# Performance work log

Hardware: AMD Instinct MI355X
Metric: run time of the kernel (lower is better)

The kernel has to match this reference:

```python
import jax, jax.numpy as jnp
import numpy as np

B, S, D_IN, H, D_HEAD = 8, 1024, 768, 12, 64

def setup_inputs() -> dict:
    key = jax.random.key(0)
    k1, k2, k3, k4 = jax.random.split(key, 4)
    x = jax.random.normal(k1, (B, S, D_IN), dtype=jnp.float32)
    # per-head projection weights, stacked: [H, d_in, d_head]
    scale = 1.0 / np.sqrt(D_IN)
    Wq = jax.random.normal(k2, (H, D_IN, D_HEAD), dtype=jnp.float32) * scale
    Wk = jax.random.normal(k3, (H, D_IN, D_HEAD), dtype=jnp.float32) * scale
    Wv = jax.random.normal(k4, (H, D_IN, D_HEAD), dtype=jnp.float32) * scale
    return {"x": x, "Wq": Wq, "Wk": Wk, "Wv": Wv}

def reference(x, Wq, Wk, Wv) -> jnp.ndarray:
    # Batched equivalent of the Python loop over heads + concat.
    q = jnp.einsum('bsd,hde->bhse', x, Wq)  # [B,H,S,Dh]
    k = jnp.einsum('bsd,hde->bhse', x, Wk)
    v = jnp.einsum('bsd,hde->bhse', x, Wv)
    scores = jnp.einsum('bhse,bhte->bhst', q, k) / jnp.sqrt(jnp.asarray(D_HEAD, x.dtype))
    causal = jnp.tril(jnp.ones((S, S), dtype=bool))  # [S,S]
    scores = jnp.where(causal, scores, jnp.asarray(-jnp.inf, x.dtype))
    attn = jax.nn.softmax(scores, axis=-1)  # dropout p=0.0 -> identity
    ctx = jnp.einsum('bhst,bhte->bhse', attn, v)  # [B,H,S,Dh]
    # concat heads along last dim -> [B,S,H*Dh]
    return jnp.transpose(ctx, (0, 2, 1, 3)).reshape(B, S, H * D_HEAD)
```

## Files before the change

kernel.cpp:

```cpp
#include <hip/hip_runtime.h>

typedef short short8 __attribute__((ext_vector_type(8)));
typedef float f32x4 __attribute__((ext_vector_type(4)));
typedef float f32x16 __attribute__((ext_vector_type(16)));

#define SQ   1024
#define DIN  768
#define NH   12
#define DH   64
#define SCL2 0.1803368801111243f

static __device__ __forceinline__ ushort f2bf(float f) {
  union { float f; unsigned u; } v; v.f = f;
  unsigned u = v.u;
  unsigned r = (u + 0x7FFFu + ((u >> 16) & 1u)) >> 16;
  return (ushort)r;
}
static __device__ __forceinline__ unsigned cvtpk(float a, float b) {
  unsigned r;
  asm("v_cvt_pk_bf16_f32 %0, %1, %2" : "=v"(r) : "v"(a), "v"(b));
  return r;
}

static __device__ __forceinline__ void gload_lds16(const ushort* g, ushort* l) {
  __builtin_amdgcn_global_load_lds(
      (const __attribute__((address_space(1))) unsigned*)(g),
      (__attribute__((address_space(3))) unsigned*)(l),
      16, 0, 0);
}

__global__ __launch_bounds__(256) void k_convert_x(const float* __restrict__ x,
                                                   ushort* __restrict__ xb) {
  int i = (blockIdx.x * 256 + threadIdx.x) * 8;
  float4 v0 = *reinterpret_cast<const float4*>(x + i);
  float4 v1 = *reinterpret_cast<const float4*>(x + i + 4);
  uint4 o;
  o.x = cvtpk(v0.x, v0.y); o.y = cvtpk(v0.z, v0.w);
  o.z = cvtpk(v1.x, v1.y); o.w = cvtpk(v1.z, v1.w);
  *reinterpret_cast<uint4*>(xb + i) = o;
}

__global__ __launch_bounds__(256) void k_prep_w(const float* __restrict__ Wq,
                                                const float* __restrict__ Wk,
                                                const float* __restrict__ Wv,
                                                ushort* __restrict__ wt) {
  __shared__ ushort tile[64][65];
  const int mh = blockIdx.x;
  const int m = mh / 12, h = mh % 12;
  const int d0 = blockIdx.y * 64;
  const float* W = (m == 0 ? Wq : (m == 1 ? Wk : Wv)) + h * DIN * DH;
  ushort* outp = wt + (size_t)mh * DH * DIN;
  #pragma unroll
  for (int p = 0; p < 16; ++p) {
    int idx = p * 256 + threadIdx.x;
    int d = idx >> 6, e = idx & 63;
    tile[d][e] = f2bf(W[(d0 + d) * DH + e]);
  }
  __syncthreads();
  #pragma unroll
  for (int p = 0; p < 16; ++p) {
    int idx = p * 256 + threadIdx.x;
    int e = idx >> 6, d = idx & 63;
    outp[e * DIN + d0 + d] = tile[d][e];
  }
}

__global__ __launch_bounds__(256, 2) void k_proj(const ushort* __restrict__ xb,
                                                 const ushort* __restrict__ wt,
                                                 ushort* __restrict__ qo,
                                                 ushort* __restrict__ ko,
                                                 ushort* __restrict__ vto) {
  __shared__ __align__(16) ushort Sb[24576];

  const int brow = blockIdx.x * 256;
  const int bn   = blockIdx.y * 128;
  const int w    = threadIdx.x >> 6, lane = threadIdx.x & 63;
  const int lr   = lane & 15, lg = lane >> 4;
  const int wm   = w >> 1, wn = w & 1;

  const int srow  = threadIdx.x >> 2;
  const int sslot = (threadIdx.x & 3) ^ (srow & 3) ^ ((srow >> 2) & 3);
  const ushort* gA = xb + (size_t)(brow + srow) * DIN + sslot * 8;
  const ushort* gB = wt + (size_t)(bn   + srow) * DIN + sslot * 8;

  f32x4 acc[8][4];
  #pragma unroll
  for (int i = 0; i < 8; ++i)
    #pragma unroll
    for (int j = 0; j < 4; ++j) acc[i][j] = (f32x4){0.f, 0.f, 0.f, 0.f};

  const int fr   = (lr & 3) ^ ((lr >> 2) & 3);
  const int aoff = (lg ^ fr) * 8;

#define STAGEP(bi, tt) do {                                               \
    const int k0_ = (tt) * 32;                                            \
    ushort* la_ = Sb + (bi) * 8192 + threadIdx.x * 8;                     \
    ushort* lb_ = Sb + 16384 + (bi) * 4096 + threadIdx.x * 8;             \
    gload_lds16(gA + k0_,             la_);                               \
    gload_lds16(gA + k0_ +  64 * DIN, la_ + 2048);                        \
    gload_lds16(gA + k0_ + 128 * DIN, la_ + 4096);                        \
    gload_lds16(gA + k0_ + 192 * DIN, la_ + 6144);                        \
    gload_lds16(gB + k0_,             lb_);                               \
    gload_lds16(gB + k0_ +  64 * DIN, lb_ + 2048);                        \
  } while (0)

  STAGEP(0, 0);
  __syncthreads();

  int cur = 0;
  #pragma unroll 1
  for (int t = 0; t < 24; ++t) {
    if (t + 1 < 24) STAGEP(cur ^ 1, t + 1);
    short8 a[8], b[4];
    #pragma unroll
    for (int mi = 0; mi < 8; ++mi)
      a[mi] = *reinterpret_cast<const short8*>(&Sb[cur * 8192 + (wm * 128 + mi * 16 + lr) * 32 + aoff]);
    #pragma unroll
    for (int ci = 0; ci < 4; ++ci)
      b[ci] = *reinterpret_cast<const short8*>(&Sb[16384 + cur * 4096 + (wn * 64 + ci * 16 + lr) * 32 + aoff]);
    #pragma unroll
    for (int mi = 0; mi < 8; ++mi)
      #pragma unroll
      for (int ci = 0; ci < 4; ++ci)
        acc[mi][ci] = __builtin_amdgcn_mfma_f32_16x16x32_bf16(a[mi], b[ci], acc[mi][ci], 0, 0, 0);
    __syncthreads();
    cur ^= 1;
  }
#undef STAGEP

  ushort* ldsw = Sb + w * 4096;
  const int mh = blockIdx.y * 2 + wn;
  const int m = mh / 12, h = mh % 12;
  const int c = lane & 7;

  #pragma unroll
  for (int p = 0; p < 2; ++p) {
    if (m < 2) {
      #pragma unroll
      for (int mi2 = 0; mi2 < 4; ++mi2)
        #pragma unroll
        for (int ci = 0; ci < 4; ++ci)
          #pragma unroll
          for (int r = 0; r < 4; ++r) {
            int sl = mi2 * 16 + lg * 4 + r;
            int e  = ci * 16 + lr;
            ldsw[sl * 64 + (e ^ ((sl & 7) << 3))] = f2bf(acc[p * 4 + mi2][ci][r]);
          }
      asm volatile("s_waitcnt lgkmcnt(0)" ::: "memory");
      ushort* dst = (m == 0) ? qo : ko;
      #pragma unroll
      for (int it = 0; it < 8; ++it) {
        int sl = it * 8 + (lane >> 3);
        short8 vv = *reinterpret_cast<const short8*>(&ldsw[sl * 64 + ((c * 8) ^ ((sl & 7) << 3))]);
        int rg = brow + wm * 128 + p * 64 + sl;
        int b_ = rg >> 10, s_ = rg & 1023;
        *reinterpret_cast<short8*>(dst + ((size_t)(b_ * 12 + h) * SQ + s_) * DH + c * 8) = vv;
      }
    } else {
      #pragma unroll
      for (int mi2 = 0; mi2 < 4; ++mi2)
        #pragma unroll
        for (int ci = 0; ci < 4; ++ci)
          #pragma unroll
          for (int r = 0; r < 4; ++r) {
            int sl = mi2 * 16 + lg * 4 + r;
            int e  = ci * 16 + lr;
            ldsw[e * 64 + (sl ^ ((e & 7) << 3))] = f2bf(acc[p * 4 + mi2][ci][r]);
          }
      asm volatile("s_waitcnt lgkmcnt(0)" ::: "memory");
      #pragma unroll
      for (int it = 0; it < 8; ++it) {
        int e = it * 8 + (lane >> 3);
        short8 vv = *reinterpret_cast<const short8*>(&ldsw[e * 64 + ((c * 8) ^ ((e & 7) << 3))]);
        int rg = brow + wm * 128 + p * 64 + c * 8;
        int b_ = rg >> 10, s_ = rg & 1023;
        *reinterpret_cast<short8*>(vto + ((size_t)(b_ * 12 + h) * DH + e) * SQ + s_) = vv;
      }
    }
  }
}

__global__ __launch_bounds__(256, 3) void k_attn(const ushort* __restrict__ qi,
                                                 const ushort* __restrict__ ki,
                                                 const ushort* __restrict__ vti,
                                                 float* __restrict__ out) {
  __shared__ __align__(16) ushort Kb[2][64 * 64];
  __shared__ __align__(16) ushort Vb[2][64 * 64];

  const int f = blockIdx.x;
  const int g = f >> 8, r_ = f & 255;
  const int qt = ((r_ & 7) + g * 3) & 7;
  const int bh = g * 32 + (r_ >> 3);
  const int b = bh / 12, h = bh % 12;
  const int w = threadIdx.x >> 6, lane = threadIdx.x & 63;
  const int ql = lane & 31, hi = lane >> 5;
  const int q0 = qt * 128 + w * 32;
  const int nt = (q0 >> 6) + 1;
  const int ntmax = 2 * qt + 2;
  const ushort* qb = qi  + (size_t)bh * SQ * DH;
  const ushort* kb = ki  + (size_t)bh * SQ * DH;
  const ushort* vb = vti + (size_t)bh * DH * SQ;

  short8 qf[4];
  #pragma unroll
  for (int m = 0; m < 4; ++m)
    qf[m] = *reinterpret_cast<const short8*>(qb + (size_t)(q0 + ql) * DH + m * 16 + hi * 8);

  f32x16 o0, o1;
  #pragma unroll
  for (int r = 0; r < 16; ++r) { o0[r] = 0.f; o1[r] = 0.f; }
  float m_run = -1e30f, l_run = 0.f;

#define STAGE(bufi, tt) do {                                                                   \
    const int kv0_ = (tt) * 64;                                                                \
    const int t0 = threadIdx.x, t1 = threadIdx.x + 256;                                        \
    gload_lds16(kb + (size_t)(kv0_ + (t0 >> 3)) * DH + (((t0 & 7) ^ ((t0 >> 3) & 7)) * 8),     \
                &Kb[bufi][0] + t0 * 8);                                                        \
    gload_lds16(kb + (size_t)(kv0_ + (t1 >> 3)) * DH + (((t1 & 7) ^ ((t1 >> 3) & 7)) * 8),     \
                &Kb[bufi][0] + t1 * 8);                                                        \
    gload_lds16(vb + (size_t)(t0 >> 3) * SQ + kv0_ + (((t0 & 7) ^ ((t0 >> 3) & 7)) * 8),       \
                &Vb[bufi][0] + t0 * 8);                                                        \
    gload_lds16(vb + (size_t)(t1 >> 3) * SQ + kv0_ + (((t1 & 7) ^ ((t1 >> 3) & 7)) * 8),       \
                &Vb[bufi][0] + t1 * 8);                                                        \
  } while (0)

  STAGE(0, 0);
  __syncthreads();

  int cur = 0;
  #pragma unroll 1
  for (int t = 0; t < ntmax; ++t) {
    if (t + 1 < ntmax) STAGE(cur ^ 1, t + 1);

    if (t < nt) {
      const int kv0 = t * 64;
      const ushort* Kc = &Kb[cur][0];
      const ushort* Vc = &Vb[cur][0];

      f32x16 s0, s1;
      #pragma unroll
      for (int r = 0; r < 16; ++r) { s0[r] = 0.f; s1[r] = 0.f; }
      #pragma unroll
      for (int m = 0; m < 4; ++m) {
        short8 kf = *reinterpret_cast<const short8*>(Kc + ql * 64 + ((2 * m + hi) ^ (ql & 7)) * 8);
        s0 = __builtin_amdgcn_mfma_f32_32x32x16_bf16(kf, qf[m], s0, 0, 0, 0);
      }
      #pragma unroll
      for (int m = 0; m < 4; ++m) {
        short8 kf = *reinterpret_cast<const short8*>(Kc + (32 + ql) * 64 + ((2 * m + hi) ^ (ql & 7)) * 8);
        s1 = __builtin_amdgcn_mfma_f32_32x32x16_bf16(kf, qf[m], s1, 0, 0, 0);
      }

      if (t == nt - 1) {
        const int qg = q0 + ql;
        #pragma unroll
        for (int r = 0; r < 16; ++r) {
          int kvl = (r & 3) + 8 * (r >> 2) + 4 * hi;
          if (kv0 + kvl      > qg) s0[r] = -1e30f;
          if (kv0 + 32 + kvl > qg) s1[r] = -1e30f;
        }
      }

      float mt = s0[0];
      #pragma unroll
      for (int r = 1; r < 16; ++r) mt = fmaxf(mt, s0[r]);
      #pragma unroll
      for (int r = 0; r < 16; ++r) mt = fmaxf(mt, s1[r]);
      mt = fmaxf(mt, __shfl_xor(mt, 32));
      if (__any(mt > m_run + 40.0f)) {
        float mnew = fmaxf(m_run, mt);
        float corr = exp2f((m_run - mnew) * SCL2);
        l_run *= corr; m_run = mnew;
        #pragma unroll
        for (int r = 0; r < 16; ++r) {
          float cr = __shfl(corr, (r & 3) + 8 * (r >> 2) + 4 * hi);
          o0[r] *= cr; o1[r] *= cr;
        }
      }
      float ts = 0.f;
      #pragma unroll
      for (int r = 0; r < 16; ++r) {
        s0[r] = exp2f((s0[r] - m_run) * SCL2); ts += s0[r];
        s1[r] = exp2f((s1[r] - m_run) * SCL2); ts += s1[r];
      }
      ts += __shfl_xor(ts, 32);
      l_run += ts;

#define PV_CHUNK(SV, CC, KC) do {                                                              \
        unsigned wa = cvtpk(SV[(CC) * 8 + 0], SV[(CC) * 8 + 1]);                               \
        unsigned wb = cvtpk(SV[(CC) * 8 + 2], SV[(CC) * 8 + 3]);                               \
        unsigned wc = cvtpk(SV[(CC) * 8 + 4], SV[(CC) * 8 + 5]);                               \
        unsigned wd = cvtpk(SV[(CC) * 8 + 6], SV[(CC) * 8 + 7]);                               \
        unsigned xa = __shfl_xor(wa, 32), xb2 = __shfl_xor(wb, 32);                            \
        unsigned xc = __shfl_xor(wc, 32), xd = __shfl_xor(wd, 32);                             \
        uint4 pw;                                                                              \
        pw.x = hi ? xc : wa;  pw.y = hi ? xd : wb;                                             \
        pw.z = hi ? wc : xa;  pw.w = hi ? wd : xb2;                                            \
        short8 pa = *reinterpret_cast<short8*>(&pw);                                           \
        short8 vf0 = *reinterpret_cast<const short8*>(Vc + ql * 64 +                           \
                       ((2 * (KC) + hi) ^ (ql & 7)) * 8);                                      \
        o0 = __builtin_amdgcn_mfma_f32_32x32x16_bf16(pa, vf0, o0, 0, 0, 0);                    \
        short8 vf1 = *reinterpret_cast<const short8*>(Vc + (32 + ql) * 64 +                    \
                       ((2 * (KC) + hi) ^ (ql & 7)) * 8);                                      \
        o1 = __builtin_amdgcn_mfma_f32_32x32x16_bf16(pa, vf1, o1, 0, 0, 0);                    \
      } while (0)

      PV_CHUNK(s0, 0, 0);
      PV_CHUNK(s0, 1, 1);
      PV_CHUNK(s1, 0, 2);
      PV_CHUNK(s1, 1, 3);
#undef PV_CHUNK
    }

    __syncthreads();
    cur ^= 1;
  }
#undef STAGE

  float rl = 1.0f / l_run;
  #pragma unroll
  for (int r = 0; r < 16; ++r) {
    int base = (r & 3) + 8 * (r >> 2) + 4 * hi;
    float sc_ = __shfl(rl, base);
    int qg = q0 + base;
    float* op = out + ((size_t)b * SQ + qg) * (NH * DH) + h * DH;
    op[ql]      = o0[r] * sc_;
    op[32 + ql] = o1[r] * sc_;
  }
}

extern "C" void kernel_launch(void* const* d_in, const int* in_sizes, int n_in,
                              void* d_out, int out_size, void* d_ws, size_t ws_size,
                              hipStream_t stream) {
  const float* x  = (const float*)d_in[0];
  const float* Wq = (const float*)d_in[1];
  const float* Wk = (const float*)d_in[2];
  const float* Wv = (const float*)d_in[3];
  float* out = (float*)d_out;

  char* ws = (char*)d_ws;
  ushort* xb = (ushort*)(ws);
  ushort* wt = (ushort*)(ws + 12582912);
  ushort* q  = (ushort*)(ws + 16121856);
  ushort* k  = (ushort*)(ws + 28704768);
  ushort* vt = (ushort*)(ws + 41287680);

  k_convert_x<<<3072, 256, 0, stream>>>(x, xb);
  k_prep_w<<<dim3(36, 12), 256, 0, stream>>>(Wq, Wk, Wv, wt);
  k_proj<<<dim3(32, 18), 256, 0, stream>>>(xb, wt, q, k, vt);
  k_attn<<<768, 256, 0, stream>>>(q, k, vt, out);
}
```

Before: 171.3 us.

## Restructure projection GEMM: 128-row tiles, 32x32 MFMA, triple-buffered LDS pipeline

The projection GEMM tile shrinks from 256x128 to 128x128, which doubles the grid to 64x18 blocks for better CU fill. The inner product moves from 16x16x32 to 32x32x16 MFMA instructions. The LDS double buffer becomes a three-stage ring that prefetches two steps ahead, gated by vmcnt waits and a single barrier per iteration. Smaller tiles give less operand reuse per block and more global traffic, traded for more parallelism and latency hiding.

Measured after the change: 169.7 us. About the same (-1.0%).

```diff
diff --git a/kernel.cpp b/kernel.cpp
--- a/kernel.cpp
+++ b/kernel.cpp
@@ -65,17 +65,17 @@
   }
 }
 
-__global__ __launch_bounds__(256, 2) void k_proj(const ushort* __restrict__ xb,
-                                                 const ushort* __restrict__ wt,
-                                                 ushort* __restrict__ qo,
-                                                 ushort* __restrict__ ko,
-                                                 ushort* __restrict__ vto) {
+__global__ __launch_bounds__(256) void k_proj(const ushort* __restrict__ xb,
+                                              const ushort* __restrict__ wt,
+                                              ushort* __restrict__ qo,
+                                              ushort* __restrict__ ko,
+                                              ushort* __restrict__ vto) {
   __shared__ __align__(16) ushort Sb[24576];
 
-  const int brow = blockIdx.x * 256;
+  const int brow = blockIdx.x * 128;
   const int bn   = blockIdx.y * 128;
   const int w    = threadIdx.x >> 6, lane = threadIdx.x & 63;
-  const int lr   = lane & 15, lg = lane >> 4;
+  const int ql   = lane & 31, hi = lane >> 5;
   const int wm   = w >> 1, wn = w & 1;
 
   const int srow  = threadIdx.x >> 2;
@@ -83,99 +83,116 @@
   const ushort* gA = xb + (size_t)(brow + srow) * DIN + sslot * 8;
   const ushort* gB = wt + (size_t)(bn   + srow) * DIN + sslot * 8;
 
-  f32x4 acc[8][4];
-  #pragma unroll
-  for (int i = 0; i < 8; ++i)
-    #pragma unroll
-    for (int j = 0; j < 4; ++j) acc[i][j] = (f32x4){0.f, 0.f, 0.f, 0.f};
-
-  const int fr   = (lr & 3) ^ ((lr >> 2) & 3);
-  const int aoff = (lg ^ fr) * 8;
+  f32x16 acc[2][2];
+  #pragma unroll
+  for (int i = 0; i < 2; ++i)
+    #pragma unroll
+    for (int j = 0; j < 2; ++j)
+      #pragma unroll
+      for (int r = 0; r < 16; ++r) acc[i][j][r] = 0.f;
+
+  const int frq = (ql & 3) ^ ((ql >> 2) & 3);
 
 #define STAGEP(bi, tt) do {                                               \
     const int k0_ = (tt) * 32;                                            \
-    ushort* la_ = Sb + (bi) * 8192 + threadIdx.x * 8;                     \
-    ushort* lb_ = Sb + 16384 + (bi) * 4096 + threadIdx.x * 8;             \
-    gload_lds16(gA + k0_,             la_);                               \
-    gload_lds16(gA + k0_ +  64 * DIN, la_ + 2048);                        \
-    gload_lds16(gA + k0_ + 128 * DIN, la_ + 4096);                        \
-    gload_lds16(gA + k0_ + 192 * DIN, la_ + 6144);                        \
-    gload_lds16(gB + k0_,             lb_);                               \
-    gload_lds16(gB + k0_ +  64 * DIN, lb_ + 2048);                        \
+    ushort* la_ = Sb + (bi) * 4096 + threadIdx.x * 8;                     \
+    ushort* lb_ = Sb + 12288 + (bi) * 4096 + threadIdx.x * 8;             \
+    gload_lds16(gA + k0_,            la_);                                \
+    gload_lds16(gA + k0_ + 64 * DIN, la_ + 2048);                         \
+    gload_lds16(gB + k0_,            lb_);                                \
+    gload_lds16(gB + k0_ + 64 * DIN, lb_ + 2048);                         \
   } while (0)
 
   STAGEP(0, 0);
-  __syncthreads();
+  STAGEP(1, 1);
 
   int cur = 0;
   #pragma unroll 1
   for (int t = 0; t < 24; ++t) {
-    if (t + 1 < 24) STAGEP(cur ^ 1, t + 1);
-    short8 a[8], b[4];
-    #pragma unroll
-    for (int mi = 0; mi < 8; ++mi)
-      a[mi] = *reinterpret_cast<const short8*>(&Sb[cur * 8192 + (wm * 128 + mi * 16 + lr) * 32 + aoff]);
-    #pragma unroll
-    for (int ci = 0; ci < 4; ++ci)
-      b[ci] = *reinterpret_cast<const short8*>(&Sb[16384 + cur * 4096 + (wn * 64 + ci * 16 + lr) * 32 + aoff]);
-    #pragma unroll
-    for (int mi = 0; mi < 8; ++mi)
-      #pragma unroll
-      for (int ci = 0; ci < 4; ++ci)
-        acc[mi][ci] = __builtin_amdgcn_mfma_f32_16x16x32_bf16(a[mi], b[ci], acc[mi][ci], 0, 0, 0);
-    __syncthreads();
-    cur ^= 1;
+    if (t < 23) asm volatile("s_waitcnt vmcnt(4)" ::: "memory");
+    else        asm volatile("s_waitcnt vmcnt(0)" ::: "memory");
+    __builtin_amdgcn_sched_barrier(0);
+    __builtin_amdgcn_s_barrier();
+    __builtin_amdgcn_sched_barrier(0);
+    if (t + 2 < 24) {
+      int nb = cur + 2; if (nb >= 3) nb -= 3;
+      STAGEP(nb, t + 2);
+    }
+    short8 a[2][2], b[2][2];
+    #pragma unroll
+    for (int ai = 0; ai < 2; ++ai) {
+      const int row = wm * 64 + ai * 32 + ql;
+      #pragma unroll
+      for (int ks = 0; ks < 2; ++ks)
+        a[ai][ks] = *reinterpret_cast<const short8*>(
+            &Sb[cur * 4096 + row * 32 + (((ks * 2 + hi) ^ frq) * 8)]);
+    }
+    #pragma unroll
+    for (int ci = 0; ci < 2; ++ci) {
+      const int row = wn * 64 + ci * 32 + ql;
+      #pragma unroll
+      for (int ks = 0; ks < 2; ++ks)
+        b[ci][ks] = *reinterpret_cast<const short8*>(
+            &Sb[12288 + cur * 4096 + row * 32 + (((ks * 2 + hi) ^ frq) * 8)]);
+    }
+    #pragma unroll
+    for (int ai = 0; ai < 2; ++ai)
+      #pragma unroll
+      for (int ci = 0; ci < 2; ++ci) {
+        acc[ai][ci] = __builtin_amdgcn_mfma_f32_32x32x16_bf16(a[ai][0], b[ci][0], acc[ai][ci], 0, 0, 0);
+        acc[ai][ci] = __builtin_amdgcn_mfma_f32_32x32x16_bf16(a[ai][1], b[ci][1], acc[ai][ci], 0, 0, 0);
+      }
+    cur += 1; if (cur >= 3) cur = 0;
   }
 #undef STAGEP
+
+  __syncthreads();
 
   ushort* ldsw = Sb + w * 4096;
   const int mh = blockIdx.y * 2 + wn;
   const int m = mh / 12, h = mh % 12;
   const int c = lane & 7;
 
-  #pragma unroll
-  for (int p = 0; p < 2; ++p) {
-    if (m < 2) {
-      #pragma unroll
-      for (int mi2 = 0; mi2 < 4; ++mi2)
+  if (m < 2) {
+    #pragma unroll
+    for (int ai = 0; ai < 2; ++ai)
+      #pragma unroll
+      for (int ci = 0; ci < 2; ++ci)
         #pragma unroll
-        for (int ci = 0; ci < 4; ++ci)
-          #pragma unroll
-          for (int r = 0; r < 4; ++r) {
-            int sl = mi2 * 16 + lg * 4 + r;
-            int e  = ci * 16 + lr;
-            ldsw[sl * 64 + (e ^ ((sl & 7) << 3))] = f2bf(acc[p * 4 + mi2][ci][r]);
-          }
-      asm volatile("s_waitcnt lgkmcnt(0)" ::: "memory");
-      ushort* dst = (m == 0) ? qo : ko;
-      #pragma unroll
-      for (int it = 0; it < 8; ++it) {
-        int sl = it * 8 + (lane >> 3);
-        short8 vv = *reinterpret_cast<const short8*>(&ldsw[sl * 64 + ((c * 8) ^ ((sl & 7) << 3))]);
-        int rg = brow + wm * 128 + p * 64 + sl;
-        int b_ = rg >> 10, s_ = rg & 1023;
-        *reinterpret_cast<short8*>(dst + ((size_t)(b_ * 12 + h) * SQ + s_) * DH + c * 8) = vv;
-      }
-    } else {
-      #pragma unroll
-      for (int mi2 = 0; mi2 < 4; ++mi2)
+        for (int r = 0; r < 16; ++r) {
+          int sl = ai * 32 + (r & 3) + 8 * (r >> 2) + 4 * hi;
+          int e  = ci * 32 + ql;
+          ldsw[sl * 64 + (e ^ ((sl & 7) << 3))] = f2bf(acc[ai][ci][r]);
+        }
+    asm volatile("s_waitcnt lgkmcnt(0)" ::: "memory");
+    ushort* dst = (m == 0) ? qo : ko;
+    #pragma unroll
+    for (int it = 0; it < 8; ++it) {
+      int sl = it * 8 + (lane >> 3);
+      short8 vv = *reinterpret_cast<const short8*>(&ldsw[sl * 64 + ((c * 8) ^ ((sl & 7) << 3))]);
+      int rg = brow + wm * 64 + sl;
+      int b_ = rg >> 10, s_ = rg & 1023;
+      *reinterpret_cast<short8*>(dst + ((size_t)(b_ * 12 + h) * SQ + s_) * DH + c * 8) = vv;
+    }
+  } else {
+    #pragma unroll
+    for (int ai = 0; ai < 2; ++ai)
+      #pragma unroll
+      for (int ci = 0; ci < 2; ++ci)
         #pragma unroll
-        for (int ci = 0; ci < 4; ++ci)
-          #pragma unroll
-          for (int r = 0; r < 4; ++r) {
-            int sl = mi2 * 16 + lg * 4 + r;
-            int e  = ci * 16 + lr;
-            ldsw[e * 64 + (sl ^ ((e & 7) << 3))] = f2bf(acc[p * 4 + mi2][ci][r]);
-          }
-      asm volatile("s_waitcnt lgkmcnt(0)" ::: "memory");
-      #pragma unroll
-      for (int it = 0; it < 8; ++it) {
-        int e = it * 8 + (lane >> 3);
-        short8 vv = *reinterpret_cast<const short8*>(&ldsw[e * 64 + ((c * 8) ^ ((e & 7) << 3))]);
-        int rg = brow + wm * 128 + p * 64 + c * 8;
-        int b_ = rg >> 10, s_ = rg & 1023;
-        *reinterpret_cast<short8*>(vto + ((size_t)(b_ * 12 + h) * DH + e) * SQ + s_) = vv;
-      }
+        for (int r = 0; r < 16; ++r) {
+          int sl = ai * 32 + (r & 3) + 8 * (r >> 2) + 4 * hi;
+          int e  = ci * 32 + ql;
+          ldsw[e * 64 + (sl ^ ((e & 7) << 3))] = f2bf(acc[ai][ci][r]);
+        }
+    asm volatile("s_waitcnt lgkmcnt(0)" ::: "memory");
+    #pragma unroll
+    for (int it = 0; it < 8; ++it) {
+      int e = it * 8 + (lane >> 3);
+      short8 vv = *reinterpret_cast<const short8*>(&ldsw[e * 64 + ((c * 8) ^ ((e & 7) << 3))]);
+      int rg = brow + wm * 64 + c * 8;
+      int b_ = rg >> 10, s_ = rg & 1023;
+      *reinterpret_cast<short8*>(vto + ((size_t)(b_ * 12 + h) * DH + e) * SQ + s_) = vv;
     }
   }
 }
@@ -347,6 +364,6 @@
 
   k_convert_x<<<3072, 256, 0, stream>>>(x, xb);
   k_prep_w<<<dim3(36, 12), 256, 0, stream>>>(Wq, Wk, Wv, wt);
-  k_proj<<<dim3(32, 18), 256, 0, stream>>>(xb, wt, q, k, vt);
+  k_proj<<<dim3(64, 18), 256, 0, stream>>>(xb, wt, q, k, vt);
   k_attn<<<768, 256, 0, stream>>>(q, k, vt, out);
 }
```
